# Kernel tuning notes

Measured on AMD Instinct MI355X. Metric: run time of the kernel, lower is better.

## Reference

```python
import jax, jax.numpy as jnp
import numpy as np

TOP_P = 0.9
NEG_FILL = -1000000000.0


def _top_p_mask(logits):
    # probabilities over vocab
    probs = jax.nn.softmax(logits, axis=-1)
    # sort descending; keep the permutation to scatter the mask back
    order = jnp.argsort(-probs, axis=-1)                      # [B, V]
    ordered = jnp.take_along_axis(probs, order, axis=-1)      # [B, V]
    cum = jnp.cumsum(ordered, axis=-1)
    cum = cum.at[..., -1].set(0.0)
    cum = jnp.roll(cum, shift=1, axis=-1)                     # exclusive cumsum
    cmask = cum <= TOP_P                                      # [B, V] in sorted order
    # scatter back: selection[b, order[b, j]] = cmask[b, j]  <=>  gather by inverse perm
    inv = jnp.argsort(order, axis=-1)
    return jnp.take_along_axis(cmask, inv, axis=-1)


def setup_inputs() -> dict:
    key = jax.random.key(0)
    k1, k2 = jax.random.split(key)
    B, V = 256, 128000
    logits = jax.random.normal(k1, (B, V), dtype=jnp.float32)
    u = jax.random.uniform(k2, (B,), dtype=jnp.float32)
    return {"logits": logits, "u": u, "temperature": 1}


def reference(logits, u, temperature):
    t = jnp.asarray(temperature, dtype=logits.dtype)
    logits = logits / t
    sel = _top_p_mask(logits)
    masked = jnp.where(sel, logits, jnp.asarray(NEG_FILL, logits.dtype))
    probs = jax.nn.softmax(masked, axis=-1)                   # [B, V]
    # multinomial(num_samples=1) via inverse-CDF with uniform u
    cdf = jnp.cumsum(probs, axis=-1)
    token = jnp.sum(cdf < u[:, None], axis=-1)
    return jnp.minimum(token, probs.shape[-1] - 1)
```

## Files before the change

### kernel.cpp

```cpp
#include <hip/hip_runtime.h>

#define BLOCK 1024
#define NW (BLOCK / 64)
#define FPSCALE 8192.0f
#define INVSCALE 0x1p-13f

__device__ __forceinline__ float wincl(float v, int lane) {
#pragma unroll
    for (int o = 1; o < 64; o <<= 1) {
        float x = __shfl_up(v, o, 64);
        if (lane >= o) v += x;
    }
    return v;
}

__device__ __forceinline__ void find_crit_desc(const float* h, int n, int seg,
                                               float limit, int lane, int* out_b) {
    float segsum = 0.f;
    int start = n - 1 - lane * seg;
    for (int k = 0; k < seg; k++) segsum += h[start - k];
    float incl = wincl(segsum, lane);
    unsigned long long mk = __ballot(incl > limit);
    if (mk == 0ULL) { *out_b = 0; return; }
    int fl = __ffsll(mk) - 1;
    float base = __shfl(incl, fl, 64) - __shfl(segsum, fl, 64);
    int sstart = n - 1 - fl * seg;
    float v = (lane < seg) ? h[sstart - lane] : 0.f;
    float incl2 = wincl(v, lane);
    unsigned long long mk2 = __ballot((lane < seg) && (base + incl2 > limit));
    int k2 = mk2 ? (__ffsll(mk2) - 1) : (seg - 1);
    *out_b = sstart - k2;
}

#define OKEY(bb) ((bb) ^ ((unsigned)((int)(bb) >> 31) | 0x80000000u))

#define LD4(j) (*(const float4*)(row + (j)))

#define P1(xx) { unsigned kk = OKEY(__float_as_uint(xx)); \
                 float e = __expf((xx) * inv_t); \
                 atomicAdd(&histbuf[((kk >> 21) << 2) | rep], \
                           (unsigned)(e * FPSCALE + 0.5f)); }

#define P2(xx, ss) { unsigned kk = OKEY(__float_as_uint(xx)); \
                     float e = __expf((xx) * inv_t); \
                     if (kk >= Tlow) ss += e; }

__global__ __launch_bounds__(BLOCK, 8) void ns_hist(
    const float* __restrict__ logits, const int* __restrict__ temp,
    unsigned* __restrict__ part, int Vv) {
    const int bid = blockIdx.x;
    const int b = bid >> 1, h = bid & 1;
    const float* __restrict__ row = logits + (size_t)b * (size_t)Vv;
    const int t = threadIdx.x;
    const int rep = t & 3;

    __shared__ __align__(16) unsigned histbuf[8192];

    const float inv_t = 1.0f / (float)temp[0];
    const int S = BLOCK * 4;
    const int HL = (((Vv + 1) >> 1) + 3) & ~3;
    const int lo = h * HL;
    const int hi = min(Vv, lo + HL);
    const int hi4 = (hi > lo) ? lo + ((hi - lo) & ~3) : lo;

    for (int i = t; i < 8192; i += BLOCK) histbuf[i] = 0u;
    __syncthreads();

    {
        int i = lo + t * 4;
        for (; i + 3 * S + 3 < hi4; i += 4 * S) {
            float4 a = LD4(i), b4 = LD4(i + S), c = LD4(i + 2 * S), d = LD4(i + 3 * S);
            P1(a.x); P1(a.y); P1(a.z); P1(a.w);
            P1(b4.x); P1(b4.y); P1(b4.z); P1(b4.w);
            P1(c.x); P1(c.y); P1(c.z); P1(c.w);
            P1(d.x); P1(d.y); P1(d.z); P1(d.w);
        }
        for (; i + 3 < hi4; i += S) { float4 a = LD4(i); P1(a.x); P1(a.y); P1(a.z); P1(a.w); }
        for (int j = hi4 + t; j < hi; j += BLOCK) P1(row[j]);
    }
    __syncthreads();

    unsigned* __restrict__ dst = part + (size_t)bid * 2048;
    for (int i = t; i < 2048; i += BLOCK) {
        uint4 m4 = *(const uint4*)&histbuf[i << 2];
        dst[i] = m4.x + m4.y + m4.z + m4.w;
    }
}

__global__ __launch_bounds__(BLOCK) void ns_walk(
    const unsigned* __restrict__ part, unsigned* __restrict__ tlow, int Bn) {
    const int b = blockIdx.x;
    const int t = threadIdx.x;
    const int lane = t & 63;
    const int wave = t >> 6;

    __shared__ float mg[2048];
    __shared__ float sweep[NW];

    const unsigned* __restrict__ pa = part + (size_t)(b * 2) * 2048;
    const unsigned* __restrict__ pb = part + (size_t)(b * 2 + 1) * 2048;

    float zp = 0.f;
    for (int i = t; i < 2048; i += BLOCK) {
        float m = (float)(pa[i] + pb[i]) * INVSCALE;
        mg[i] = m;
        zp += m;
    }
#pragma unroll
    for (int o = 32; o >= 1; o >>= 1) zp += __shfl_xor(zp, o, 64);
    if (lane == 0) sweep[wave] = zp;
    __syncthreads();
    float Z = 0.f;
    for (int w = 0; w < NW; w++) Z += sweep[w];
    const float limit = 0.9f * Z;

    if (wave == 0) {
        int b1w;
        find_crit_desc(mg, 2048, 32, limit, lane, &b1w);
        if (lane == 0) tlow[b] = (unsigned)b1w << 21;
    }
}

__global__ __launch_bounds__(BLOCK, 8) void ns_csum(
    const float* __restrict__ logits, const int* __restrict__ temp,
    const unsigned* __restrict__ tlow, float* __restrict__ csum, int Vv) {
    const int bid = blockIdx.x;
    const int b = bid >> 1, h = bid & 1;
    const float* __restrict__ row = logits + (size_t)b * (size_t)Vv;
    const int t = threadIdx.x;
    const int lane = t & 63;
    const int wave = t >> 6;

    const float inv_t = 1.0f / (float)temp[0];
    const unsigned Tlow = tlow[b];
    const int nch = (Vv + 1023) >> 10;
    const int nchh = (nch + 1) >> 1;
    const int clo = h * nchh;
    const int chi = min(nch, clo + nchh);
    float* __restrict__ cs = csum + (size_t)b * 128;

    for (int c0 = clo + wave; c0 < chi; c0 += 2 * NW) {
        const int c1 = c0 + NW;
        const bool haveB = (c1 < chi);
        float s0 = 0.f, s1 = 0.f;
        const int bA = c0 << 10, bB = c1 << 10;
        if (bA + 1024 <= Vv && (!haveB || bB + 1024 <= Vv)) {
            float4 a0 = LD4(bA + lane * 4);
            float4 a1 = LD4(bA + 256 + lane * 4);
            float4 a2 = LD4(bA + 512 + lane * 4);
            float4 a3 = LD4(bA + 768 + lane * 4);
            if (haveB) {
                float4 b0 = LD4(bB + lane * 4);
                float4 b1v = LD4(bB + 256 + lane * 4);
                float4 b2 = LD4(bB + 512 + lane * 4);
                float4 b3 = LD4(bB + 768 + lane * 4);
                P2(b0.x, s1); P2(b0.y, s1); P2(b0.z, s1); P2(b0.w, s1);
                P2(b1v.x, s1); P2(b1v.y, s1); P2(b1v.z, s1); P2(b1v.w, s1);
                P2(b2.x, s1); P2(b2.y, s1); P2(b2.z, s1); P2(b2.w, s1);
                P2(b3.x, s1); P2(b3.y, s1); P2(b3.z, s1); P2(b3.w, s1);
            }
            P2(a0.x, s0); P2(a0.y, s0); P2(a0.z, s0); P2(a0.w, s0);
            P2(a1.x, s0); P2(a1.y, s0); P2(a1.z, s0); P2(a1.w, s0);
            P2(a2.x, s0); P2(a2.y, s0); P2(a2.z, s0); P2(a2.w, s0);
            P2(a3.x, s0); P2(a3.y, s0); P2(a3.z, s0); P2(a3.w, s0);
        } else {
            for (int q = 0; q < 16; q++) {
                int i = bA + (q << 6) + lane;
                if (i < Vv) { float x = row[i]; P2(x, s0); }
            }
            if (haveB) {
                for (int q = 0; q < 16; q++) {
                    int i = bB + (q << 6) + lane;
                    if (i < Vv) { float x = row[i]; P2(x, s1); }
                }
            }
        }
#pragma unroll
        for (int o = 32; o >= 1; o >>= 1) s0 += __shfl_xor(s0, o, 64);
        if (lane == 0) cs[c0] = s0;
        if (haveB) {
#pragma unroll
            for (int o = 32; o >= 1; o >>= 1) s1 += __shfl_xor(s1, o, 64);
            if (lane == 0) cs[c1] = s1;
        }
    }
}

__global__ __launch_bounds__(64) void ns_pick(
    const float* __restrict__ logits, const float* __restrict__ uvec,
    const int* __restrict__ temp, const unsigned* __restrict__ tlow,
    const float* __restrict__ csum, int* __restrict__ out, int Vv) {
    const int b = blockIdx.x;
    const float* __restrict__ row = logits + (size_t)b * (size_t)Vv;
    const int lane = threadIdx.x;
    const float inv_t = 1.0f / (float)temp[0];
    const unsigned Tlow = tlow[b];
    const int nch = (Vv + 1023) >> 10;
    const float* __restrict__ cs = csum + (size_t)b * 128;

    float c0v = (2 * lane < nch) ? cs[2 * lane] : 0.f;
    float c1v = (2 * lane + 1 < nch) ? cs[2 * lane + 1] : 0.f;
    float segsum = c0v + c1v;
    float incl = wincl(segsum, lane);
    float total = __shfl(incl, 63, 64);
    const float U = uvec[b] * total;
    unsigned long long mk = __ballot(incl >= U);
    int token;
    if (mk == 0ULL) {
        token = Vv;
    } else {
        int fl = __ffsll(mk) - 1;
        float base = __shfl(incl, fl, 64) - __shfl(segsum, fl, 64);
        float v = (lane < 2 && fl * 2 + lane < nch) ? cs[fl * 2 + lane] : 0.f;
        float incl2 = wincl(v, lane);
        unsigned long long mk2 = __ballot((lane < 2) && (base + incl2 >= U));
        int k2i = mk2 ? (__ffsll(mk2) - 1) : 1;
        int cx = fl * 2 + k2i;
        float B = base + __shfl(incl2, k2i, 64) - __shfl(v, k2i, 64);
        int cb = cx << 10;
        float vv[16];
#pragma unroll
        for (int r = 0; r < 16; r++) {
            int idx = cb + r * 64 + lane;
            vv[r] = (idx < Vv) ? row[idx] : -1e30f;
        }
        int cnt2 = 0;
#pragma unroll
        for (int r = 0; r < 16; r++) {
            int idx = cb + r * 64 + lane;
            unsigned kk = OKEY(__float_as_uint(vv[r]));
            float e = __expf(vv[r] * inv_t);
            float keep = (kk >= Tlow) ? e : 0.f;
            float is = wincl(keep, lane);
            unsigned long long mm = __ballot((idx < Vv) && (B + is < U));
            cnt2 += __popcll(mm);
            B += __shfl(is, 63, 64);
        }
        token = cb + cnt2;
    }
    if (lane == 0) out[b] = (token < Vv - 1) ? token : (Vv - 1);
}

__global__ __launch_bounds__(BLOCK) void NucleusSampling_79336635892529_kernel(
    const float* __restrict__ logits, const float* __restrict__ uvec,
    const int* __restrict__ temp, int* __restrict__ out, int Vv) {
    const int b = blockIdx.x;
    const float* __restrict__ row = logits + (size_t)b * (size_t)Vv;
    const int t = threadIdx.x;
    const int lane = t & 63;
    const int wave = t >> 6;
    const int rep = lane & 3;

    __shared__ __align__(16) unsigned histbuf[8192];
    __shared__ float mg[2048];
    __shared__ float sweep[NW];
    __shared__ float csum[128];
    __shared__ int shb1;

    const float inv_t = 1.0f / (float)temp[0];
    const int V4 = Vv & ~3;
    const int S = BLOCK * 4;
    const int nch = (Vv + 1023) >> 10;

    for (int i = t; i < 8192; i += BLOCK) histbuf[i] = 0u;
    __syncthreads();
    {
        int i = t * 4;
        for (; i + 3 * S + 3 < V4; i += 4 * S) {
            float4 a = LD4(i), b4 = LD4(i + S), c = LD4(i + 2 * S), d = LD4(i + 3 * S);
            P1(a.x); P1(a.y); P1(a.z); P1(a.w);
            P1(b4.x); P1(b4.y); P1(b4.z); P1(b4.w);
            P1(c.x); P1(c.y); P1(c.z); P1(c.w);
            P1(d.x); P1(d.y); P1(d.z); P1(d.w);
        }
        for (; i < V4; i += S) { float4 a = LD4(i); P1(a.x); P1(a.y); P1(a.z); P1(a.w); }
        for (int j = V4 + t; j < Vv; j += BLOCK) P1(row[j]);
    }
    __syncthreads();
    float zp = 0.f;
    for (int i = t; i < 2048; i += BLOCK) {
        uint4 m4 = *(const uint4*)&histbuf[i << 2];
        float m = (float)(m4.x + m4.y + m4.z + m4.w) * INVSCALE;
        mg[i] = m;
        zp += m;
    }
#pragma unroll
    for (int o = 32; o >= 1; o >>= 1) zp += __shfl_xor(zp, o, 64);
    if (lane == 0) sweep[wave] = zp;
    __syncthreads();
    float Z = 0.f;
    for (int w = 0; w < NW; w++) Z += sweep[w];
    const float limit = 0.9f * Z;
    if (wave == 0) {
        int b1w;
        find_crit_desc(mg, 2048, 32, limit, lane, &b1w);
        if (lane == 0) shb1 = b1w;
    }
    if (t < 128 && t >= nch) csum[t] = 0.f;
    __syncthreads();
    const unsigned Tlow = (unsigned)shb1 << 21;

    for (int c0 = wave; c0 < nch; c0 += 2 * NW) {
        const int c1 = c0 + NW;
        const bool haveB = (c1 < nch);
        float s0 = 0.f, s1 = 0.f;
        const int bA = c0 << 10, bB = c1 << 10;
        if (bA + 1024 <= Vv && (!haveB || bB + 1024 <= Vv)) {
            float4 a0 = LD4(bA + lane * 4);
            float4 a1 = LD4(bA + 256 + lane * 4);
            float4 a2 = LD4(bA + 512 + lane * 4);
            float4 a3 = LD4(bA + 768 + lane * 4);
            if (haveB) {
                float4 b0 = LD4(bB + lane * 4);
                float4 b1v = LD4(bB + 256 + lane * 4);
                float4 b2 = LD4(bB + 512 + lane * 4);
                float4 b3 = LD4(bB + 768 + lane * 4);
                P2(b0.x, s1); P2(b0.y, s1); P2(b0.z, s1); P2(b0.w, s1);
                P2(b1v.x, s1); P2(b1v.y, s1); P2(b1v.z, s1); P2(b1v.w, s1);
                P2(b2.x, s1); P2(b2.y, s1); P2(b2.z, s1); P2(b2.w, s1);
                P2(b3.x, s1); P2(b3.y, s1); P2(b3.z, s1); P2(b3.w, s1);
            }
            P2(a0.x, s0); P2(a0.y, s0); P2(a0.z, s0); P2(a0.w, s0);
            P2(a1.x, s0); P2(a1.y, s0); P2(a1.z, s0); P2(a1.w, s0);
            P2(a2.x, s0); P2(a2.y, s0); P2(a2.z, s0); P2(a2.w, s0);
            P2(a3.x, s0); P2(a3.y, s0); P2(a3.z, s0); P2(a3.w, s0);
        } else {
            for (int q = 0; q < 16; q++) {
                int i = bA + (q << 6) + lane;
                if (i < Vv) { float x = row[i]; P2(x, s0); }
            }
            if (haveB) {
                for (int q = 0; q < 16; q++) {
                    int i = bB + (q << 6) + lane;
                    if (i < Vv) { float x = row[i]; P2(x, s1); }
                }
            }
        }
#pragma unroll
        for (int o = 32; o >= 1; o >>= 1) s0 += __shfl_xor(s0, o, 64);
        if (lane == 0) csum[c0] = s0;
        if (haveB) {
#pragma unroll
            for (int o = 32; o >= 1; o >>= 1) s1 += __shfl_xor(s1, o, 64);
            if (lane == 0) csum[c1] = s1;
        }
    }
    __syncthreads();

    if (wave == 0) {
        float segsum = csum[lane * 2] + csum[lane * 2 + 1];
        float incl = wincl(segsum, lane);
        float total = __shfl(incl, 63, 64);
        const float U = uvec[b] * total;
        unsigned long long mk = __ballot(incl >= U);
        int token;
        if (mk == 0ULL) {
            token = Vv;
        } else {
            int fl = __ffsll(mk) - 1;
            float base = __shfl(incl, fl, 64) - __shfl(segsum, fl, 64);
            float v = (lane < 2) ? csum[fl * 2 + lane] : 0.f;
            float incl2 = wincl(v, lane);
            unsigned long long mk2 = __ballot((lane < 2) && (base + incl2 >= U));
            int k2i = mk2 ? (__ffsll(mk2) - 1) : 1;
            int cx = fl * 2 + k2i;
            float B = base + __shfl(incl2, k2i, 64) - __shfl(v, k2i, 64);
            int cb = cx << 10;
            float vv[16];
#pragma unroll
            for (int r = 0; r < 16; r++) {
                int idx = cb + r * 64 + lane;
                vv[r] = (idx < Vv) ? row[idx] : -1e30f;
            }
            int cnt2 = 0;
#pragma unroll
            for (int r = 0; r < 16; r++) {
                int idx = cb + r * 64 + lane;
                unsigned kk = OKEY(__float_as_uint(vv[r]));
                float e = __expf(vv[r] * inv_t);
                float keep = (kk >= Tlow) ? e : 0.f;
                float is = wincl(keep, lane);
                unsigned long long mm = __ballot((idx < Vv) && (B + is < U));
                cnt2 += __popcll(mm);
                B += __shfl(is, 63, 64);
            }
            token = cb + cnt2;
        }
        if (lane == 0) out[b] = (token < Vv - 1) ? token : (Vv - 1);
    }
}

extern "C" void kernel_launch(void* const* d_in, const int* in_sizes, int n_in,
                              void* d_out, int out_size, void* d_ws, size_t ws_size,
                              hipStream_t stream) {
    const float* logits = (const float*)d_in[0];
    const float* u = (const float*)d_in[1];
    const int* temp = (const int*)d_in[2];
    int* out = (int*)d_out;
    int B = in_sizes[1];
    int V = in_sizes[0] / B;

    size_t sz_hist = (size_t)B * 2 * 2048 * sizeof(unsigned);
    size_t off_tlow = sz_hist;
    size_t sz_tlow = ((size_t)B * sizeof(unsigned) + 255) & ~(size_t)255;
    size_t off_csum = off_tlow + sz_tlow;
    size_t need = off_csum + (size_t)B * 128 * sizeof(float);

    if (d_ws != nullptr && ws_size >= need) {
        unsigned* part = (unsigned*)d_ws;
        unsigned* tlow = (unsigned*)((char*)d_ws + off_tlow);
        float* csum = (float*)((char*)d_ws + off_csum);
        ns_hist<<<2 * B, BLOCK, 0, stream>>>(logits, temp, part, V);
        ns_walk<<<B, BLOCK, 0, stream>>>(part, tlow, B);
        ns_csum<<<2 * B, BLOCK, 0, stream>>>(logits, temp, tlow, csum, V);
        ns_pick<<<B, 64, 0, stream>>>(logits, u, temp, tlow, csum, out, V);
    } else {
        NucleusSampling_79336635892529_kernel<<<B, BLOCK, 0, stream>>>(
            logits, u, temp, out, V);
    }
}
```

Measured before the change: 222.6 us.

## Fuse walk, chunk-sum and pick into one per-row kernel after histogram

Replaces three kernels (threshold walk, chunk partial sums over two half-row blocks, single-wave pick) with one block-per-row kernel that finds the threshold, computes the 1024-element chunk sums into shared memory, and does the inverse-CDF pick. This removes two launches and the global round-trips for tlow and csum. The cost is that the second pass over the row now uses one block per row instead of two, which halves the parallelism for that read. It also drops the occupancy hint of 8 from the histogram kernel's launch bounds.

```diff
diff --git a/kernel.cpp b/kernel.cpp
--- a/kernel.cpp
+++ b/kernel.cpp
@@ -45,7 +45,7 @@
                      float e = __expf((xx) * inv_t); \
                      if (kk >= Tlow) ss += e; }
 
-__global__ __launch_bounds__(BLOCK, 8) void ns_hist(
+__global__ __launch_bounds__(BLOCK) void ns_hist(
     const float* __restrict__ logits, const int* __restrict__ temp,
     unsigned* __restrict__ part, int Vv) {
     const int bid = blockIdx.x;
@@ -87,15 +87,23 @@
     }
 }
 
-__global__ __launch_bounds__(BLOCK) void ns_walk(
-    const unsigned* __restrict__ part, unsigned* __restrict__ tlow, int Bn) {
+__global__ __launch_bounds__(BLOCK) void ns_rest(
+    const float* __restrict__ logits, const float* __restrict__ uvec,
+    const int* __restrict__ temp, const unsigned* __restrict__ part,
+    int* __restrict__ out, int Vv) {
     const int b = blockIdx.x;
+    const float* __restrict__ row = logits + (size_t)b * (size_t)Vv;
     const int t = threadIdx.x;
     const int lane = t & 63;
     const int wave = t >> 6;
 
     __shared__ float mg[2048];
     __shared__ float sweep[NW];
+    __shared__ float csum[128];
+    __shared__ int shb1;
+
+    const float inv_t = 1.0f / (float)temp[0];
+    const int nch = (Vv + 1023) >> 10;
 
     const unsigned* __restrict__ pa = part + (size_t)(b * 2) * 2048;
     const unsigned* __restrict__ pb = part + (size_t)(b * 2 + 1) * 2048;
@@ -114,183 +122,6 @@
     for (int w = 0; w < NW; w++) Z += sweep[w];
     const float limit = 0.9f * Z;
 
-    if (wave == 0) {
-        int b1w;
-        find_crit_desc(mg, 2048, 32, limit, lane, &b1w);
-        if (lane == 0) tlow[b] = (unsigned)b1w << 21;
-    }
-}
-
-__global__ __launch_bounds__(BLOCK, 8) void ns_csum(
-    const float* __restrict__ logits, const int* __restrict__ temp,
-    const unsigned* __restrict__ tlow, float* __restrict__ csum, int Vv) {
-    const int bid = blockIdx.x;
-    const int b = bid >> 1, h = bid & 1;
-    const float* __restrict__ row = logits + (size_t)b * (size_t)Vv;
-    const int t = threadIdx.x;
-    const int lane = t & 63;
-    const int wave = t >> 6;
-
-    const float inv_t = 1.0f / (float)temp[0];
-    const unsigned Tlow = tlow[b];
-    const int nch = (Vv + 1023) >> 10;
-    const int nchh = (nch + 1) >> 1;
-    const int clo = h * nchh;
-    const int chi = min(nch, clo + nchh);
-    float* __restrict__ cs = csum + (size_t)b * 128;
-
-    for (int c0 = clo + wave; c0 < chi; c0 += 2 * NW) {
-        const int c1 = c0 + NW;
-        const bool haveB = (c1 < chi);
-        float s0 = 0.f, s1 = 0.f;
-        const int bA = c0 << 10, bB = c1 << 10;
-        if (bA + 1024 <= Vv && (!haveB || bB + 1024 <= Vv)) {
-            float4 a0 = LD4(bA + lane * 4);
-            float4 a1 = LD4(bA + 256 + lane * 4);
-            float4 a2 = LD4(bA + 512 + lane * 4);
-            float4 a3 = LD4(bA + 768 + lane * 4);
-            if (haveB) {
-                float4 b0 = LD4(bB + lane * 4);
-                float4 b1v = LD4(bB + 256 + lane * 4);
-                float4 b2 = LD4(bB + 512 + lane * 4);
-                float4 b3 = LD4(bB + 768 + lane * 4);
-                P2(b0.x, s1); P2(b0.y, s1); P2(b0.z, s1); P2(b0.w, s1);
-                P2(b1v.x, s1); P2(b1v.y, s1); P2(b1v.z, s1); P2(b1v.w, s1);
-                P2(b2.x, s1); P2(b2.y, s1); P2(b2.z, s1); P2(b2.w, s1);
-                P2(b3.x, s1); P2(b3.y, s1); P2(b3.z, s1); P2(b3.w, s1);
-            }
-            P2(a0.x, s0); P2(a0.y, s0); P2(a0.z, s0); P2(a0.w, s0);
-            P2(a1.x, s0); P2(a1.y, s0); P2(a1.z, s0); P2(a1.w, s0);
-            P2(a2.x, s0); P2(a2.y, s0); P2(a2.z, s0); P2(a2.w, s0);
-            P2(a3.x, s0); P2(a3.y, s0); P2(a3.z, s0); P2(a3.w, s0);
-        } else {
-            for (int q = 0; q < 16; q++) {
-                int i = bA + (q << 6) + lane;
-                if (i < Vv) { float x = row[i]; P2(x, s0); }
-            }
-            if (haveB) {
-                for (int q = 0; q < 16; q++) {
-                    int i = bB + (q << 6) + lane;
-                    if (i < Vv) { float x = row[i]; P2(x, s1); }
-                }
-            }
-        }
-#pragma unroll
-        for (int o = 32; o >= 1; o >>= 1) s0 += __shfl_xor(s0, o, 64);
-        if (lane == 0) cs[c0] = s0;
-        if (haveB) {
-#pragma unroll
-            for (int o = 32; o >= 1; o >>= 1) s1 += __shfl_xor(s1, o, 64);
-            if (lane == 0) cs[c1] = s1;
-        }
-    }
-}
-
-__global__ __launch_bounds__(64) void ns_pick(
-    const float* __restrict__ logits, const float* __restrict__ uvec,
-    const int* __restrict__ temp, const unsigned* __restrict__ tlow,
-    const float* __restrict__ csum, int* __restrict__ out, int Vv) {
-    const int b = blockIdx.x;
-    const float* __restrict__ row = logits + (size_t)b * (size_t)Vv;
-    const int lane = threadIdx.x;
-    const float inv_t = 1.0f / (float)temp[0];
-    const unsigned Tlow = tlow[b];
-    const int nch = (Vv + 1023) >> 10;
-    const float* __restrict__ cs = csum + (size_t)b * 128;
-
-    float c0v = (2 * lane < nch) ? cs[2 * lane] : 0.f;
-    float c1v = (2 * lane + 1 < nch) ? cs[2 * lane + 1] : 0.f;
-    float segsum = c0v + c1v;
-    float incl = wincl(segsum, lane);
-    float total = __shfl(incl, 63, 64);
-    const float U = uvec[b] * total;
-    unsigned long long mk = __ballot(incl >= U);
-    int token;
-    if (mk == 0ULL) {
-        token = Vv;
-    } else {
-        int fl = __ffsll(mk) - 1;
-        float base = __shfl(incl, fl, 64) - __shfl(segsum, fl, 64);
-        float v = (lane < 2 && fl * 2 + lane < nch) ? cs[fl * 2 + lane] : 0.f;
-        float incl2 = wincl(v, lane);
-        unsigned long long mk2 = __ballot((lane < 2) && (base + incl2 >= U));
-        int k2i = mk2 ? (__ffsll(mk2) - 1) : 1;
-        int cx = fl * 2 + k2i;
-        float B = base + __shfl(incl2, k2i, 64) - __shfl(v, k2i, 64);
-        int cb = cx << 10;
-        float vv[16];
-#pragma unroll
-        for (int r = 0; r < 16; r++) {
-            int idx = cb + r * 64 + lane;
-            vv[r] = (idx < Vv) ? row[idx] : -1e30f;
-        }
-        int cnt2 = 0;
-#pragma unroll
-        for (int r = 0; r < 16; r++) {
-            int idx = cb + r * 64 + lane;
-            unsigned kk = OKEY(__float_as_uint(vv[r]));
-            float e = __expf(vv[r] * inv_t);
-            float keep = (kk >= Tlow) ? e : 0.f;
-            float is = wincl(keep, lane);
-            unsigned long long mm = __ballot((idx < Vv) && (B + is < U));
-            cnt2 += __popcll(mm);
-            B += __shfl(is, 63, 64);
-        }
-        token = cb + cnt2;
-    }
-    if (lane == 0) out[b] = (token < Vv - 1) ? token : (Vv - 1);
-}
-
-__global__ __launch_bounds__(BLOCK) void NucleusSampling_79336635892529_kernel(
-    const float* __restrict__ logits, const float* __restrict__ uvec,
-    const int* __restrict__ temp, int* __restrict__ out, int Vv) {
-    const int b = blockIdx.x;
-    const float* __restrict__ row = logits + (size_t)b * (size_t)Vv;
-    const int t = threadIdx.x;
-    const int lane = t & 63;
-    const int wave = t >> 6;
-    const int rep = lane & 3;
-
-    __shared__ __align__(16) unsigned histbuf[8192];
-    __shared__ float mg[2048];
-    __shared__ float sweep[NW];
-    __shared__ float csum[128];
-    __shared__ int shb1;
-
-    const float inv_t = 1.0f / (float)temp[0];
-    const int V4 = Vv & ~3;
-    const int S = BLOCK * 4;
-    const int nch = (Vv + 1023) >> 10;
-
-    for (int i = t; i < 8192; i += BLOCK) histbuf[i] = 0u;
-    __syncthreads();
-    {
-        int i = t * 4;
-        for (; i + 3 * S + 3 < V4; i += 4 * S) {
-            float4 a = LD4(i), b4 = LD4(i + S), c = LD4(i + 2 * S), d = LD4(i + 3 * S);
-            P1(a.x); P1(a.y); P1(a.z); P1(a.w);
-            P1(b4.x); P1(b4.y); P1(b4.z); P1(b4.w);
-            P1(c.x); P1(c.y); P1(c.z); P1(c.w);
-            P1(d.x); P1(d.y); P1(d.z); P1(d.w);
-        }
-        for (; i < V4; i += S) { float4 a = LD4(i); P1(a.x); P1(a.y); P1(a.z); P1(a.w); }
-        for (int j = V4 + t; j < Vv; j += BLOCK) P1(row[j]);
-    }
-    __syncthreads();
-    float zp = 0.f;
-    for (int i = t; i < 2048; i += BLOCK) {
-        uint4 m4 = *(const uint4*)&histbuf[i << 2];
-        float m = (float)(m4.x + m4.y + m4.z + m4.w) * INVSCALE;
-        mg[i] = m;
-        zp += m;
-    }
-#pragma unroll
-    for (int o = 32; o >= 1; o >>= 1) zp += __shfl_xor(zp, o, 64);
-    if (lane == 0) sweep[wave] = zp;
-    __syncthreads();
-    float Z = 0.f;
-    for (int w = 0; w < NW; w++) Z += sweep[w];
-    const float limit = 0.9f * Z;
     if (wave == 0) {
         int b1w;
         find_crit_desc(mg, 2048, 32, limit, lane, &b1w);
@@ -390,6 +221,155 @@
     }
 }
 
+__global__ __launch_bounds__(BLOCK) void NucleusSampling_79336635892529_kernel(
+    const float* __restrict__ logits, const float* __restrict__ uvec,
+    const int* __restrict__ temp, int* __restrict__ out, int Vv) {
+    const int b = blockIdx.x;
+    const float* __restrict__ row = logits + (size_t)b * (size_t)Vv;
+    const int t = threadIdx.x;
+    const int lane = t & 63;
+    const int wave = t >> 6;
+    const int rep = lane & 3;
+
+    __shared__ __align__(16) unsigned histbuf[8192];
+    __shared__ float mg[2048];
+    __shared__ float sweep[NW];
+    __shared__ float csum[128];
+    __shared__ int shb1;
+
+    const float inv_t = 1.0f / (float)temp[0];
+    const int V4 = Vv & ~3;
+    const int S = BLOCK * 4;
+    const int nch = (Vv + 1023) >> 10;
+
+    for (int i = t; i < 8192; i += BLOCK) histbuf[i] = 0u;
+    __syncthreads();
+    {
+        int i = t * 4;
+        for (; i + 3 * S + 3 < V4; i += 4 * S) {
+            float4 a = LD4(i), b4 = LD4(i + S), c = LD4(i + 2 * S), d = LD4(i + 3 * S);
+            P1(a.x); P1(a.y); P1(a.z); P1(a.w);
+            P1(b4.x); P1(b4.y); P1(b4.z); P1(b4.w);
+            P1(c.x); P1(c.y); P1(c.z); P1(c.w);
+            P1(d.x); P1(d.y); P1(d.z); P1(d.w);
+        }
+        for (; i < V4; i += S) { float4 a = LD4(i); P1(a.x); P1(a.y); P1(a.z); P1(a.w); }
+        for (int j = V4 + t; j < Vv; j += BLOCK) P1(row[j]);
+    }
+    __syncthreads();
+    float zp = 0.f;
+    for (int i = t; i < 2048; i += BLOCK) {
+        uint4 m4 = *(const uint4*)&histbuf[i << 2];
+        float m = (float)(m4.x + m4.y + m4.z + m4.w) * INVSCALE;
+        mg[i] = m;
+        zp += m;
+    }
+#pragma unroll
+    for (int o = 32; o >= 1; o >>= 1) zp += __shfl_xor(zp, o, 64);
+    if (lane == 0) sweep[wave] = zp;
+    __syncthreads();
+    float Z = 0.f;
+    for (int w = 0; w < NW; w++) Z += sweep[w];
+    const float limit = 0.9f * Z;
+    if (wave == 0) {
+        int b1w;
+        find_crit_desc(mg, 2048, 32, limit, lane, &b1w);
+        if (lane == 0) shb1 = b1w;
+    }
+    if (t < 128 && t >= nch) csum[t] = 0.f;
+    __syncthreads();
+    const unsigned Tlow = (unsigned)shb1 << 21;
+
+    for (int c0 = wave; c0 < nch; c0 += 2 * NW) {
+        const int c1 = c0 + NW;
+        const bool haveB = (c1 < nch);
+        float s0 = 0.f, s1 = 0.f;
+        const int bA = c0 << 10, bB = c1 << 10;
+        if (bA + 1024 <= Vv && (!haveB || bB + 1024 <= Vv)) {
+            float4 a0 = LD4(bA + lane * 4);
+            float4 a1 = LD4(bA + 256 + lane * 4);
+            float4 a2 = LD4(bA + 512 + lane * 4);
+            float4 a3 = LD4(bA + 768 + lane * 4);
+            if (haveB) {
+                float4 b0 = LD4(bB + lane * 4);
+                float4 b1v = LD4(bB + 256 + lane * 4);
+                float4 b2 = LD4(bB + 512 + lane * 4);
+                float4 b3 = LD4(bB + 768 + lane * 4);
+                P2(b0.x, s1); P2(b0.y, s1); P2(b0.z, s1); P2(b0.w, s1);
+                P2(b1v.x, s1); P2(b1v.y, s1); P2(b1v.z, s1); P2(b1v.w, s1);
+                P2(b2.x, s1); P2(b2.y, s1); P2(b2.z, s1); P2(b2.w, s1);
+                P2(b3.x, s1); P2(b3.y, s1); P2(b3.z, s1); P2(b3.w, s1);
+            }
+            P2(a0.x, s0); P2(a0.y, s0); P2(a0.z, s0); P2(a0.w, s0);
+            P2(a1.x, s0); P2(a1.y, s0); P2(a1.z, s0); P2(a1.w, s0);
+            P2(a2.x, s0); P2(a2.y, s0); P2(a2.z, s0); P2(a2.w, s0);
+            P2(a3.x, s0); P2(a3.y, s0); P2(a3.z, s0); P2(a3.w, s0);
+        } else {
+            for (int q = 0; q < 16; q++) {
+                int i = bA + (q << 6) + lane;
+                if (i < Vv) { float x = row[i]; P2(x, s0); }
+            }
+            if (haveB) {
+                for (int q = 0; q < 16; q++) {
+                    int i = bB + (q << 6) + lane;
+                    if (i < Vv) { float x = row[i]; P2(x, s1); }
+                }
+            }
+        }
+#pragma unroll
+        for (int o = 32; o >= 1; o >>= 1) s0 += __shfl_xor(s0, o, 64);
+        if (lane == 0) csum[c0] = s0;
+        if (haveB) {
+#pragma unroll
+            for (int o = 32; o >= 1; o >>= 1) s1 += __shfl_xor(s1, o, 64);
+            if (lane == 0) csum[c1] = s1;
+        }
+    }
+    __syncthreads();
+
+    if (wave == 0) {
+        float segsum = csum[lane * 2] + csum[lane * 2 + 1];
+        float incl = wincl(segsum, lane);
+        float total = __shfl(incl, 63, 64);
+        const float U = uvec[b] * total;
+        unsigned long long mk = __ballot(incl >= U);
+        int token;
+        if (mk == 0ULL) {
+            token = Vv;
+        } else {
+            int fl = __ffsll(mk) - 1;
+            float base = __shfl(incl, fl, 64) - __shfl(segsum, fl, 64);
+            float v = (lane < 2) ? csum[fl * 2 + lane] : 0.f;
+            float incl2 = wincl(v, lane);
+            unsigned long long mk2 = __ballot((lane < 2) && (base + incl2 >= U));
+            int k2i = mk2 ? (__ffsll(mk2) - 1) : 1;
+            int cx = fl * 2 + k2i;
+            float B = base + __shfl(incl2, k2i, 64) - __shfl(v, k2i, 64);
+            int cb = cx << 10;
+            float vv[16];
+#pragma unroll
+            for (int r = 0; r < 16; r++) {
+                int idx = cb + r * 64 + lane;
+                vv[r] = (idx < Vv) ? row[idx] : -1e30f;
+            }
+            int cnt2 = 0;
+#pragma unroll
+            for (int r = 0; r < 16; r++) {
+                int idx = cb + r * 64 + lane;
+                unsigned kk = OKEY(__float_as_uint(vv[r]));
+                float e = __expf(vv[r] * inv_t);
+                float keep = (kk >= Tlow) ? e : 0.f;
+                float is = wincl(keep, lane);
+                unsigned long long mm = __ballot((idx < Vv) && (B + is < U));
+                cnt2 += __popcll(mm);
+                B += __shfl(is, 63, 64);
+            }
+            token = cb + cnt2;
+        }
+        if (lane == 0) out[b] = (token < Vv - 1) ? token : (Vv - 1);
+    }
+}
+
 extern "C" void kernel_launch(void* const* d_in, const int* in_sizes, int n_in,
                               void* d_out, int out_size, void* d_ws, size_t ws_size,
                               hipStream_t stream) {
@@ -400,20 +380,11 @@
     int B = in_sizes[1];
     int V = in_sizes[0] / B;
 
-    size_t sz_hist = (size_t)B * 2 * 2048 * sizeof(unsigned);
-    size_t off_tlow = sz_hist;
-    size_t sz_tlow = ((size_t)B * sizeof(unsigned) + 255) & ~(size_t)255;
-    size_t off_csum = off_tlow + sz_tlow;
-    size_t need = off_csum + (size_t)B * 128 * sizeof(float);
-
+    size_t need = (size_t)B * 2 * 2048 * sizeof(unsigned);
     if (d_ws != nullptr && ws_size >= need) {
         unsigned* part = (unsigned*)d_ws;
-        unsigned* tlow = (unsigned*)((char*)d_ws + off_tlow);
-        float* csum = (float*)((char*)d_ws + off_csum);
         ns_hist<<<2 * B, BLOCK, 0, stream>>>(logits, temp, part, V);
-        ns_walk<<<B, BLOCK, 0, stream>>>(part, tlow, B);
-        ns_csum<<<2 * B, BLOCK, 0, stream>>>(logits, temp, tlow, csum, V);
-        ns_pick<<<B, 64, 0, stream>>>(logits, u, temp, tlow, csum, out, V);
+        ns_rest<<<B, BLOCK, 0, stream>>>(logits, u, temp, part, out, V);
     } else {
         NucleusSampling_79336635892529_kernel<<<B, BLOCK, 0, stream>>>(
             logits, u, temp, out, V);
```

After: 216.4 us. -2.8%, faster.
